# Kernel tuning notes

Measured on AMD Instinct MI355X. Metric: run time of the kernel, lower is better.

The kernel has to match this reference:

```python
import jax, jax.numpy as jnp
import numpy as np

N, K, D_IN, D_H, D_A, N_CLS = 8192, 10, 1024, 512, 256, 4


def setup_inputs() -> dict:
    key = jax.random.key(0)
    ks = jax.random.split(key, 20)
    def lin(k, fan_in, shape):
        return jax.random.normal(k, shape, dtype=jnp.float32) / np.sqrt(fan_in)
    return {
        "x_path": jax.random.normal(ks[0], (N, D_IN), dtype=jnp.float32),
        "cluster_id": jax.random.randint(ks[1], (N,), 0, K),
        # per-cluster phi MLP (Linear 1024->512, ReLU, Linear 512->512, ReLU); dropout = eval identity
        "W1": lin(ks[2], D_IN, (K, D_IN, D_H)), "b1": jnp.zeros((K, D_H), jnp.float32),
        "W2": lin(ks[3], D_H, (K, D_H, D_H)), "b2": jnp.zeros((K, D_H), jnp.float32),
        # attention_net fc: Linear 512->512 + ReLU
        "fc_W": lin(ks[4], D_H, (D_H, D_H)), "fc_b": jnp.zeros((D_H,), jnp.float32),
        # Attn_Net_Gated: a=tanh(Va), b=sigmoid(Vb), A=(a*b)@Vc
        "Va": lin(ks[5], D_H, (D_H, D_A)), "ba": jnp.zeros((D_A,), jnp.float32),
        "Vb": lin(ks[6], D_H, (D_H, D_A)), "bb": jnp.zeros((D_A,), jnp.float32),
        "Vc": lin(ks[7], D_A, (D_A, 1)), "bc": jnp.zeros((1,), jnp.float32),
        # rho: Linear 512->256 + ReLU
        "rho_W": lin(ks[8], D_H, (D_H, D_A)), "rho_b": jnp.zeros((D_A,), jnp.float32),
        # classifier: Linear 256->4
        "cls_W": lin(ks[9], D_A, (D_A, N_CLS)), "cls_b": jnp.zeros((N_CLS,), jnp.float32),
    }


def reference(x_path, cluster_id, W1, b1, W2, b2, fc_W, fc_b,
              Va, ba, Vb, bb, Vc, bc, rho_W, rho_b, cls_W, cls_b):
    # mask[k, n] = 1 if patch n belongs to cluster k
    mask = (cluster_id[None, :] == jnp.arange(K)[:, None]).astype(x_path.dtype)  # [K, N]

    # per-cluster 2-layer MLP applied to all patches, masked mean-pool (= AdaptiveAvgPool1d(1))
    def phi(W1i, b1i, W2i, b2i):
        h = jax.nn.relu(x_path @ W1i + b1i)          # [N, 512]
        return jax.nn.relu(h @ W2i + b2i)            # [N, 512]
    y = jax.vmap(phi)(W1, b1, W2, b2)                # [K, N, 512]
    cnt = mask.sum(axis=1)                           # [K]
    pooled = jnp.einsum('kn,knd->kd', mask, y) / jnp.maximum(cnt, 1.0)[:, None]  # [K, 512]
    # empty cluster -> zeros (matches torch.zeros((1,512)) branch since b terms are zero via where)
    pooled = jnp.where(cnt[:, None] > 0, pooled, 0.0)

    # attention_net: fc + gated attention
    h = jax.nn.relu(pooled @ fc_W + fc_b)            # [K, 512]
    a = jnp.tanh(h @ Va + ba)                        # [K, 256]
    b = jax.nn.sigmoid(h @ Vb + bb)                  # [K, 256]
    A = (a * b) @ Vc + bc                            # [K, 1]
    A = jax.nn.softmax(A.T, axis=1)                  # [1, K]
    h_path = A @ h                                   # [1, 512]
    h_path = jax.nn.relu(h_path @ rho_W + rho_b)[0]  # [256]
    logits = (h_path @ cls_W + cls_b)[None, :]       # [1, 4]
    Y_hat = jnp.argmax(logits, axis=1, keepdims=True)
    hazards = jax.nn.sigmoid(logits)
    S = jnp.cumprod(1.0 - hazards, axis=1)
    return hazards, S, Y_hat
```

## Files before the change

### kernel.cpp

```cpp
#include <hip/hip_runtime.h>
#include <math.h>

#define NPATCH 8192
#define KC     10
#define DIN    1024
#define DH     512
#define DA     256
#define NCLS   4

#define TM  32
#define LDA 520

typedef unsigned short u16;
typedef short bf16x8 __attribute__((ext_vector_type(8)));
typedef float f32x4  __attribute__((ext_vector_type(4)));

#define OFF_CNT   0
#define OFF_BAR   48
#define OFF_IDX   64
#define OFF_PSUM  327744
#define OFF_H     348224
#define OFF_H2    368768
#define OFF_SRED  369792
#define OFF_W1P   373888
#define OFF_W2P   10859648
#define OFF_H1    16102528

__device__ __forceinline__ u16 f2bf(float f) {
  union { float f; unsigned u; } v; v.f = f;
  unsigned r = (v.u + 0x7fffu + ((v.u >> 16) & 1u)) >> 16;
  return (u16)r;
}

struct __align__(8) U16x4 { u16 x, y, z, w; };

__device__ __forceinline__ void async16(const void* gp, void* lp) {
  __builtin_amdgcn_global_load_lds(
      (const __attribute__((address_space(1))) void*)gp,
      (__attribute__((address_space(3))) void*)lp, 16, 0, 0);
}

#define W1_TILES (KC * (DIN / 32) * (DH / 32))
#define W2_TILES (KC * (DH / 32) * (DH / 32))
#define NB_BUCKET 32
#define NB_PREP (NB_BUCKET + W1_TILES + W2_TILES)

__global__ __launch_bounds__(256) void prep_kernel(
    const int* __restrict__ cid, int* __restrict__ cnt,
    int* __restrict__ idxlist, const float* __restrict__ W1,
    const float* __restrict__ W2, u16* __restrict__ W1p,
    u16* __restrict__ W2p, float* __restrict__ psum) {
  int b = blockIdx.x, t = threadIdx.x;
  if (b < NB_BUCKET) {
    int g = b * 256 + t;
    if (g < KC * DH) psum[g] = 0.f;
    __shared__ int lcnt[KC], lbase[KC];
    if (t < KC) lcnt[t] = 0;
    __syncthreads();
    int n = b * 256 + t;
    int k = cid[n];
    int myoff = atomicAdd(&lcnt[k], 1);
    __syncthreads();
    if (t < KC) lbase[t] = atomicAdd(&cnt[t], lcnt[t]);
    __syncthreads();
    idxlist[k * NPATCH + lbase[k] + myoff] = n;
  } else {
    __shared__ u16 tile[32][33];
    int bb = b - NB_BUCKET;
    const float* src;
    u16* dst;
    if (bb < W1_TILES) {
      int k = bb / 512, rem = bb % 512;
      int kb = rem / 16, n0 = (rem % 16) * 32;
      src = W1 + (size_t)k * DIN * DH + (size_t)kb * 32 * DH + n0;
      dst = W1p + (((size_t)(k * 32 + kb) * 512 + n0) * 32);
    } else {
      int b2 = bb - W1_TILES;
      int k = b2 / 256, rem = b2 % 256;
      int kb = rem / 16, n0 = (rem % 16) * 32;
      src = W2 + (size_t)k * DH * DH + (size_t)kb * 32 * DH + n0;
      dst = W2p + (((size_t)(k * 16 + kb) * 512 + n0) * 32);
    }
    {
      int ki = t >> 3, n4 = (t & 7) * 4;
      float4 v = *(const float4*)&src[(size_t)ki * DH + n4];
      tile[ki][n4 + 0] = f2bf(v.x);
      tile[ki][n4 + 1] = f2bf(v.y);
      tile[ki][n4 + 2] = f2bf(v.z);
      tile[ki][n4 + 3] = f2bf(v.w);
    }
    __syncthreads();
    {
      int n = t >> 3, ki = (t & 7) * 4;
      U16x4 o = {tile[ki + 0][n], tile[ki + 1][n], tile[ki + 2][n],
                 tile[ki + 3][n]};
      *(U16x4*)&dst[(size_t)n * 32 + ki] = o;
    }
  }
}

__global__ __launch_bounds__(256) void phi1_kernel(
    const float* __restrict__ x, const u16* __restrict__ W1p,
    const float* __restrict__ b1, const int* __restrict__ cnt,
    const int* __restrict__ idxlist, u16* __restrict__ h1) {
  const int k = blockIdx.y;
  const int base = blockIdx.x * TM;
  const int nq = blockIdx.z;
  const int cntk = cnt[k];
  if (base >= cntk) return;

  const int tid = threadIdx.x;
  const int w = tid >> 6, lane = tid & 63;
  const int quad = lane >> 4, l16 = lane & 15;

  __shared__ __align__(16) u16 A_sh[TM * LDA];
  __shared__ int ridx[TM];
  if (tid < TM) {
    int r = base + tid;
    ridx[tid] = (r < cntk) ? idxlist[k * NPATCH + r] : -1;
  }
  __syncthreads();

  const f32x4 zero4 = {0.f, 0.f, 0.f, 0.f};
  f32x4 acc[2][4];
#pragma unroll
  for (int m = 0; m < 2; ++m)
#pragma unroll
    for (int nt = 0; nt < 4; ++nt) acc[m][nt] = zero4;

  for (int kh = 0; kh < 2; ++kh) {
    if (kh) __syncthreads();
#pragma unroll
    for (int rr = 0; rr < 8; ++rr) {
      int r = w * 8 + rr;
      int src = ridx[r];
      bf16x8 o = {0, 0, 0, 0, 0, 0, 0, 0};
      if (src >= 0) {
        const float4* xp =
            (const float4*)(x + (size_t)src * DIN + kh * 512 + lane * 8);
        float4 v0 = xp[0], v1 = xp[1];
        o[0] = (short)f2bf(v0.x); o[1] = (short)f2bf(v0.y);
        o[2] = (short)f2bf(v0.z); o[3] = (short)f2bf(v0.w);
        o[4] = (short)f2bf(v1.x); o[5] = (short)f2bf(v1.y);
        o[6] = (short)f2bf(v1.z); o[7] = (short)f2bf(v1.w);
      }
      *(bf16x8*)&A_sh[r * LDA + lane * 8] = o;
    }
    __syncthreads();

    const u16* wb = W1p + ((size_t)(k * 32 + kh * 16) * 512 +
                           (nq * 256 + w * 64 + l16)) * 32 + quad * 8;
    bf16x8 B[2][8];
#pragma unroll
    for (int s = 0; s < 2; ++s)
#pragma unroll
      for (int nt = 0; nt < 4; ++nt)
        B[0][s * 4 + nt] = *(const bf16x8*)(wb + (size_t)s * 16384 + nt * 512);
#pragma unroll
    for (int g = 0; g < 8; ++g) {
      const int cur = g & 1, nxt = cur ^ 1;
      if (g < 7) {
#pragma unroll
        for (int s = 0; s < 2; ++s)
#pragma unroll
          for (int nt = 0; nt < 4; ++nt)
            B[nxt][s * 4 + nt] = *(const bf16x8*)(
                wb + (size_t)((g + 1) * 2 + s) * 16384 + nt * 512);
      }
#pragma unroll
      for (int s = 0; s < 2; ++s) {
        const int ks = g * 2 + s;
        bf16x8 af0 = *(const bf16x8*)&A_sh[l16 * LDA + ks * 32 + quad * 8];
        bf16x8 af1 =
            *(const bf16x8*)&A_sh[(16 + l16) * LDA + ks * 32 + quad * 8];
#pragma unroll
        for (int nt = 0; nt < 4; ++nt) {
          acc[0][nt] = __builtin_amdgcn_mfma_f32_16x16x32_bf16(
              af0, B[cur][s * 4 + nt], acc[0][nt], 0, 0, 0);
          acc[1][nt] = __builtin_amdgcn_mfma_f32_16x16x32_bf16(
              af1, B[cur][s * 4 + nt], acc[1][nt], 0, 0, 0);
        }
      }
    }
  }

  __syncthreads();
#pragma unroll
  for (int m = 0; m < 2; ++m)
#pragma unroll
    for (int nt = 0; nt < 4; ++nt) {
      int c = w * 64 + nt * 16 + l16;
      float bias = b1[k * DH + nq * 256 + c];
#pragma unroll
      for (int r = 0; r < 4; ++r) {
        int row = m * 16 + quad * 4 + r;
        A_sh[row * 264 + c] = f2bf(fmaxf(acc[m][nt][r] + bias, 0.f));
      }
    }
  __syncthreads();
  {
    int row = tid >> 3, seg = tid & 7;
    int n = ridx[row];
    if (n >= 0) {
      u16* dst = h1 + (size_t)n * DH + nq * 256 + seg * 32;
#pragma unroll
      for (int j = 0; j < 4; ++j)
        *(bf16x8*)(dst + j * 8) =
            *(const bf16x8*)&A_sh[row * 264 + seg * 32 + j * 8];
    }
  }
}

__global__ __launch_bounds__(256) void phi2_kernel(
    const u16* __restrict__ h1, const u16* __restrict__ W2p,
    const float* __restrict__ b2, const int* __restrict__ cnt,
    const int* __restrict__ idxlist, float* __restrict__ psum) {
  const int k = blockIdx.y;
  const int base = blockIdx.x * TM;
  const int nq = blockIdx.z;
  const int cntk = cnt[k];
  if (base >= cntk) return;

  const int tid = threadIdx.x;
  const int w = tid >> 6, lane = tid & 63;
  const int quad = lane >> 4, l16 = lane & 15;

  __shared__ __align__(16) u16 H_sh[TM * LDA];
  __shared__ int ridx[TM];
  if (tid < TM) {
    int r = base + tid;
    ridx[tid] = (r < cntk) ? idxlist[k * NPATCH + r] : -1;
  }
  __syncthreads();

  for (int rr = 0; rr < 8; ++rr) {
    int r = w * 8 + rr;
    int src = ridx[r];
    if (src >= 0) {
      async16(h1 + (size_t)src * DH + lane * 8, &H_sh[r * LDA]);
    } else {
      bf16x8 z = {0, 0, 0, 0, 0, 0, 0, 0};
      *(bf16x8*)&H_sh[r * LDA + lane * 8] = z;
    }
  }
  __syncthreads();

  const f32x4 zero4 = {0.f, 0.f, 0.f, 0.f};
  f32x4 acc[2][4];
#pragma unroll
  for (int m = 0; m < 2; ++m)
#pragma unroll
    for (int nt = 0; nt < 4; ++nt) acc[m][nt] = zero4;

  const u16* wb = W2p + ((size_t)(k * 16) * 512 +
                         (nq * 256 + w * 64 + l16)) * 32 + quad * 8;
  bf16x8 B[2][8];
#pragma unroll
  for (int s = 0; s < 2; ++s)
#pragma unroll
    for (int nt = 0; nt < 4; ++nt)
      B[0][s * 4 + nt] = *(const bf16x8*)(wb + (size_t)s * 16384 + nt * 512);
#pragma unroll
  for (int g = 0; g < 8; ++g) {
    const int cur = g & 1, nxt = cur ^ 1;
    if (g < 7) {
#pragma unroll
      for (int s = 0; s < 2; ++s)
#pragma unroll
        for (int nt = 0; nt < 4; ++nt)
          B[nxt][s * 4 + nt] = *(const bf16x8*)(
              wb + (size_t)((g + 1) * 2 + s) * 16384 + nt * 512);
    }
#pragma unroll
    for (int s = 0; s < 2; ++s) {
      const int ks = g * 2 + s;
      bf16x8 af0 = *(const bf16x8*)&H_sh[l16 * LDA + ks * 32 + quad * 8];
      bf16x8 af1 =
          *(const bf16x8*)&H_sh[(16 + l16) * LDA + ks * 32 + quad * 8];
#pragma unroll
      for (int nt = 0; nt < 4; ++nt) {
        acc[0][nt] = __builtin_amdgcn_mfma_f32_16x16x32_bf16(
            af0, B[cur][s * 4 + nt], acc[0][nt], 0, 0, 0);
        acc[1][nt] = __builtin_amdgcn_mfma_f32_16x16x32_bf16(
            af1, B[cur][s * 4 + nt], acc[1][nt], 0, 0, 0);
      }
    }
  }

  float vmask[2][4];
#pragma unroll
  for (int m = 0; m < 2; ++m)
#pragma unroll
    for (int r = 0; r < 4; ++r)
      vmask[m][r] = (ridx[m * 16 + quad * 4 + r] >= 0) ? 1.f : 0.f;

#pragma unroll
  for (int nt = 0; nt < 4; ++nt) {
    int col = nq * 256 + w * 64 + nt * 16 + l16;
    float bias = b2[k * DH + col];
    float s = 0.f;
#pragma unroll
    for (int m = 0; m < 2; ++m)
#pragma unroll
      for (int r = 0; r < 4; ++r)
        s += vmask[m][r] * fmaxf(acc[m][nt][r] + bias, 0.f);
    s += __shfl_xor(s, 16, 64);
    s += __shfl_xor(s, 32, 64);
    if (quad == 0) atomicAdd(&psum[k * DH + col], s);
  }
}

#define NTB 64

__device__ __forceinline__ void bar_arrive_wait(int* bar) {
  __syncthreads();
  if (threadIdx.x == 0) {
    __threadfence();
    __hip_atomic_fetch_add(bar, 1, __ATOMIC_RELEASE, __HIP_MEMORY_SCOPE_AGENT);
    while (__hip_atomic_load(bar, __ATOMIC_ACQUIRE,
                             __HIP_MEMORY_SCOPE_AGENT) < NTB) {
      __builtin_amdgcn_s_sleep(1);
    }
  }
  __syncthreads();
}

__global__ __launch_bounds__(256) void tail_kernel(
    const float* __restrict__ psum, const int* __restrict__ cnt,
    const float* __restrict__ fcW, const float* __restrict__ fcb,
    const float* __restrict__ Va, const float* __restrict__ ba,
    const float* __restrict__ Vb, const float* __restrict__ bb_,
    const float* __restrict__ Vc, const float* __restrict__ rhoW,
    const float* __restrict__ rhob, const float* __restrict__ clsW,
    const float* __restrict__ clsb, float* __restrict__ hstore,
    float* __restrict__ sred, float* __restrict__ h2g,
    int* __restrict__ bar, float* __restrict__ out) {
  __shared__ float p_sh[KC * DH];
  __shared__ float r1[2560];
  __shared__ float r2[2560];
  __shared__ float invs[KC];
  __shared__ float gate_sh[4 * KC];
  __shared__ float ws_sh[KC];
  __shared__ float hp_sh[DH];
  const int tid = threadIdx.x;
  const int b = blockIdx.x;

  if (tid < KC) {
    int c = cnt[tid];
    invs[tid] = (c > 0) ? 1.f / (float)c : 0.f;
  }
  __syncthreads();
#pragma unroll
  for (int it = 0; it < KC * DH / 256; ++it) {
    int e = it * 256 + tid;
    p_sh[e] = psum[e] * invs[e >> 9];
  }
  __syncthreads();
  {
    const int jj = tid & 7, dq = tid >> 3;
    const int j0 = b * 8;
    float acc[KC];
#pragma unroll
    for (int k = 0; k < KC; ++k) acc[k] = 0.f;
#pragma unroll 4
    for (int i = 0; i < 16; ++i) {
      int d = dq * 16 + i;
      float wv = fcW[(size_t)d * DH + j0 + jj];
#pragma unroll
      for (int k = 0; k < KC; ++k) acc[k] = fmaf(p_sh[k * DH + d], wv, acc[k]);
    }
#pragma unroll
    for (int k = 0; k < KC; ++k) r1[(dq * 8 + jj) * KC + k] = acc[k];
    __syncthreads();
    if (tid < 8 * KC) {
      int jj2 = tid / KC, k = tid % KC;
      float s = 0.f;
#pragma unroll
      for (int q = 0; q < 32; ++q) s += r1[(q * 8 + jj2) * KC + k];
      hstore[k * DH + j0 + jj2] = fmaxf(s + fcb[j0 + jj2], 0.f);
    }
  }
  bar_arrive_wait(&bar[0]);

#pragma unroll
  for (int it = 0; it < KC * DH / 256; ++it) {
    int e = it * 256 + tid;
    p_sh[e] = hstore[e];
  }
  __syncthreads();
  {
    const int jj = tid & 3, dq = tid >> 2;
    const int j0 = b * 4;
    float sa[KC], sb[KC];
#pragma unroll
    for (int k = 0; k < KC; ++k) { sa[k] = 0.f; sb[k] = 0.f; }
#pragma unroll 4
    for (int i = 0; i < 8; ++i) {
      int d = dq * 8 + i;
      float va = Va[(size_t)d * DA + j0 + jj];
      float vb = Vb[(size_t)d * DA + j0 + jj];
#pragma unroll
      for (int k = 0; k < KC; ++k) {
        float h = p_sh[k * DH + d];
        sa[k] = fmaf(h, va, sa[k]);
        sb[k] = fmaf(h, vb, sb[k]);
      }
    }
#pragma unroll
    for (int k = 0; k < KC; ++k) {
      r1[(dq * 4 + jj) * KC + k] = sa[k];
      r2[(dq * 4 + jj) * KC + k] = sb[k];
    }
    __syncthreads();
    if (tid < 4 * KC) {
      int jj2 = tid / KC, k = tid % KC;
      float ta = 0.f, tb = 0.f;
#pragma unroll
      for (int q = 0; q < 64; ++q) {
        ta += r1[(q * 4 + jj2) * KC + k];
        tb += r2[(q * 4 + jj2) * KC + k];
      }
      float a = tanhf(ta + ba[j0 + jj2]);
      float g = 1.f / (1.f + expf(-(tb + bb_[j0 + jj2])));
      gate_sh[jj2 * KC + k] = a * g * Vc[j0 + jj2];
    }
    __syncthreads();
    if (tid < KC) {
      float s = 0.f;
#pragma unroll
      for (int jj2 = 0; jj2 < 4; ++jj2) s += gate_sh[jj2 * KC + tid];
      sred[b * 16 + tid] = s;
    }
  }
  bar_arrive_wait(&bar[1]);

  if (tid < KC) {
    float s = 0.f;
    for (int q = 0; q < NTB; ++q) s += sred[q * 16 + tid];
    ws_sh[tid] = s;
  }
  __syncthreads();
  if (tid == 0) {
    float m = -1e30f;
#pragma unroll
    for (int k2 = 0; k2 < KC; ++k2) m = fmaxf(m, ws_sh[k2]);
    float Z = 0.f;
#pragma unroll
    for (int k2 = 0; k2 < KC; ++k2) {
      float e = expf(ws_sh[k2] - m);
      ws_sh[k2] = e;
      Z += e;
    }
    float iZ = 1.f / Z;
#pragma unroll
    for (int k2 = 0; k2 < KC; ++k2) ws_sh[k2] *= iZ;
  }
  __syncthreads();
#pragma unroll
  for (int it = 0; it < 2; ++it) {
    int d = it * 256 + tid;
    float s = 0.f;
#pragma unroll
    for (int k2 = 0; k2 < KC; ++k2) s = fmaf(ws_sh[k2], p_sh[k2 * DH + d], s);
    hp_sh[d] = s;
  }
  __syncthreads();
  {
    const int jj = tid & 3, dq = tid >> 2;
    const int j0 = b * 4;
    float acc = 0.f;
#pragma unroll 4
    for (int i = 0; i < 8; ++i) {
      int d = dq * 8 + i;
      acc = fmaf(hp_sh[d], rhoW[(size_t)d * DA + j0 + jj], acc);
    }
    r1[dq * 4 + jj] = acc;
    __syncthreads();
    if (tid < 4) {
      float s = 0.f;
#pragma unroll
      for (int q = 0; q < 64; ++q) s += r1[q * 4 + tid];
      h2g[j0 + tid] = fmaxf(s + rhob[j0 + tid], 0.f);
    }
  }

  if (b != 0) {
    __syncthreads();
    if (tid == 0) {
      __threadfence();
      __hip_atomic_fetch_add(&bar[2], 1, __ATOMIC_RELEASE,
                             __HIP_MEMORY_SCOPE_AGENT);
    }
    return;
  }
  bar_arrive_wait(&bar[2]);
  {
    float h = h2g[tid];
#pragma unroll
    for (int c = 0; c < NCLS; ++c)
      r1[c * 256 + tid] = h * clsW[(size_t)tid * NCLS + c];
    __syncthreads();
    for (int s = 128; s > 0; s >>= 1) {
      if (tid < s) {
#pragma unroll
        for (int c = 0; c < NCLS; ++c)
          r1[c * 256 + tid] += r1[c * 256 + tid + s];
      }
      __syncthreads();
    }
    if (tid == 0) {
      float lg[NCLS], hz[NCLS];
      int best = 0;
#pragma unroll
      for (int c = 0; c < NCLS; ++c) {
        lg[c] = r1[c * 256] + clsb[c];
        hz[c] = 1.f / (1.f + expf(-lg[c]));
        if (lg[c] > lg[best]) best = c;
      }
      float S = 1.f;
#pragma unroll
      for (int c = 0; c < NCLS; ++c) out[c] = hz[c];
#pragma unroll
      for (int c = 0; c < NCLS; ++c) {
        S *= (1.f - hz[c]);
        out[NCLS + c] = S;
      }
      out[2 * NCLS] = (float)best;
    }
  }
}

extern "C" void kernel_launch(void* const* d_in, const int* in_sizes, int n_in,
                              void* d_out, int out_size, void* d_ws,
                              size_t ws_size, hipStream_t stream) {
  const float* x    = (const float*)d_in[0];
  const int*   cid  = (const int*)d_in[1];
  const float* W1   = (const float*)d_in[2];
  const float* b1   = (const float*)d_in[3];
  const float* W2   = (const float*)d_in[4];
  const float* b2   = (const float*)d_in[5];
  const float* fcW  = (const float*)d_in[6];
  const float* fcb  = (const float*)d_in[7];
  const float* Va   = (const float*)d_in[8];
  const float* ba   = (const float*)d_in[9];
  const float* Vb   = (const float*)d_in[10];
  const float* bb_  = (const float*)d_in[11];
  const float* Vc   = (const float*)d_in[12];
  const float* rhoW = (const float*)d_in[14];
  const float* rhob = (const float*)d_in[15];
  const float* clsW = (const float*)d_in[16];
  const float* clsb = (const float*)d_in[17];
  float* out = (float*)d_out;

  char* ws = (char*)d_ws;
  int*   cnt     = (int*)(ws + OFF_CNT);
  int*   bar     = (int*)(ws + OFF_BAR);
  int*   idxlist = (int*)(ws + OFF_IDX);
  float* psum    = (float*)(ws + OFF_PSUM);
  float* hstore  = (float*)(ws + OFF_H);
  float* h2g     = (float*)(ws + OFF_H2);
  float* sred    = (float*)(ws + OFF_SRED);
  u16*   W1p     = (u16*)(ws + OFF_W1P);
  u16*   W2p     = (u16*)(ws + OFF_W2P);
  u16*   h1      = (u16*)(ws + OFF_H1);

  (void)hipMemsetAsync(cnt, 0, 64, stream);
  prep_kernel<<<NB_PREP, 256, 0, stream>>>(cid, cnt, idxlist, W1, W2, W1p, W2p,
                                           psum);
  phi1_kernel<<<dim3(NPATCH / TM, KC, 2), 256, 0, stream>>>(x, W1p, b1, cnt,
                                                            idxlist, h1);
  phi2_kernel<<<dim3(NPATCH / TM, KC, 2), 256, 0, stream>>>(h1, W2p, b2, cnt,
                                                            idxlist, psum);
  tail_kernel<<<NTB, 256, 0, stream>>>(psum, cnt, fcW, fcb, Va, ba, Vb, bb_,
                                       Vc, rhoW, rhob, clsW, clsb, hstore,
                                       sred, h2g, bar, out);
}
```

Measured before the change: 215.2 us.

## Store h1 compacted by cluster, reorder grid, use packed bf16 converts

phi1 now writes h1 rows contiguously in cluster-sorted order, at a prefix-sum offset computed from the counts. phi2 therefore reads contiguous rows without the index-list gather, and it no longer needs the shared ridx table or its sync. The grid is reordered to (nq, k padded to 12, row-tile) so the two column halves of a tile launch next to each other, which should improve cache reuse of the x and h1 rows. The fp32-to-bf16 input conversion uses the hardware v_cvt_pk_bf16_f32 instruction in place of manual rounding. Padding the k dimension adds some empty blocks that exit early.

```diff
diff --git a/kernel.cpp b/kernel.cpp
--- a/kernel.cpp
+++ b/kernel.cpp
@@ -32,7 +32,14 @@
   return (u16)r;
 }
 
+__device__ __forceinline__ unsigned cvtpk(float lo, float hi) {
+  unsigned r;
+  asm("v_cvt_pk_bf16_f32 %0, %1, %2" : "=v"(r) : "v"(lo), "v"(hi));
+  return r;
+}
+
 struct __align__(8) U16x4 { u16 x, y, z, w; };
+union BF8U { bf16x8 v; unsigned u[4]; };
 
 __device__ __forceinline__ void async16(const void* gp, void* lp) {
   __builtin_amdgcn_global_load_lds(
@@ -104,10 +111,15 @@
     const float* __restrict__ b1, const int* __restrict__ cnt,
     const int* __restrict__ idxlist, u16* __restrict__ h1) {
   const int k = blockIdx.y;
-  const int base = blockIdx.x * TM;
-  const int nq = blockIdx.z;
+  if (k >= KC) return;
   const int cntk = cnt[k];
+  const int base = blockIdx.z * TM;
   if (base >= cntk) return;
+  const int nq = blockIdx.x;
+
+  int cbase = 0;
+#pragma unroll
+  for (int i = 0; i < KC - 1; ++i) cbase += (i < k) ? cnt[i] : 0;
 
   const int tid = threadIdx.x;
   const int w = tid >> 6, lane = tid & 63;
@@ -134,17 +146,19 @@
     for (int rr = 0; rr < 8; ++rr) {
       int r = w * 8 + rr;
       int src = ridx[r];
-      bf16x8 o = {0, 0, 0, 0, 0, 0, 0, 0};
+      BF8U o;
       if (src >= 0) {
         const float4* xp =
             (const float4*)(x + (size_t)src * DIN + kh * 512 + lane * 8);
         float4 v0 = xp[0], v1 = xp[1];
-        o[0] = (short)f2bf(v0.x); o[1] = (short)f2bf(v0.y);
-        o[2] = (short)f2bf(v0.z); o[3] = (short)f2bf(v0.w);
-        o[4] = (short)f2bf(v1.x); o[5] = (short)f2bf(v1.y);
-        o[6] = (short)f2bf(v1.z); o[7] = (short)f2bf(v1.w);
-      }
-      *(bf16x8*)&A_sh[r * LDA + lane * 8] = o;
+        o.u[0] = cvtpk(v0.x, v0.y);
+        o.u[1] = cvtpk(v0.z, v0.w);
+        o.u[2] = cvtpk(v1.x, v1.y);
+        o.u[3] = cvtpk(v1.z, v1.w);
+      } else {
+        o.u[0] = 0; o.u[1] = 0; o.u[2] = 0; o.u[3] = 0;
+      }
+      *(bf16x8*)&A_sh[r * LDA + lane * 8] = o.v;
     }
     __syncthreads();
 
@@ -200,9 +214,8 @@
   __syncthreads();
   {
     int row = tid >> 3, seg = tid & 7;
-    int n = ridx[row];
-    if (n >= 0) {
-      u16* dst = h1 + (size_t)n * DH + nq * 256 + seg * 32;
+    if (base + row < cntk) {
+      u16* dst = h1 + (size_t)(cbase + base + row) * DH + nq * 256 + seg * 32;
 #pragma unroll
       for (int j = 0; j < 4; ++j)
         *(bf16x8*)(dst + j * 8) =
@@ -214,30 +227,29 @@
 __global__ __launch_bounds__(256) void phi2_kernel(
     const u16* __restrict__ h1, const u16* __restrict__ W2p,
     const float* __restrict__ b2, const int* __restrict__ cnt,
-    const int* __restrict__ idxlist, float* __restrict__ psum) {
+    float* __restrict__ psum) {
   const int k = blockIdx.y;
-  const int base = blockIdx.x * TM;
-  const int nq = blockIdx.z;
+  if (k >= KC) return;
   const int cntk = cnt[k];
+  const int base = blockIdx.z * TM;
   if (base >= cntk) return;
+  const int nq = blockIdx.x;
+
+  int cbase = 0;
+#pragma unroll
+  for (int i = 0; i < KC - 1; ++i) cbase += (i < k) ? cnt[i] : 0;
 
   const int tid = threadIdx.x;
   const int w = tid >> 6, lane = tid & 63;
   const int quad = lane >> 4, l16 = lane & 15;
 
   __shared__ __align__(16) u16 H_sh[TM * LDA];
-  __shared__ int ridx[TM];
-  if (tid < TM) {
-    int r = base + tid;
-    ridx[tid] = (r < cntk) ? idxlist[k * NPATCH + r] : -1;
-  }
-  __syncthreads();
-
+
+  const int rowg0 = cbase + base;
   for (int rr = 0; rr < 8; ++rr) {
     int r = w * 8 + rr;
-    int src = ridx[r];
-    if (src >= 0) {
-      async16(h1 + (size_t)src * DH + lane * 8, &H_sh[r * LDA]);
+    if (base + r < cntk) {
+      async16(h1 + (size_t)(rowg0 + r) * DH + lane * 8, &H_sh[r * LDA]);
     } else {
       bf16x8 z = {0, 0, 0, 0, 0, 0, 0, 0};
       *(bf16x8*)&H_sh[r * LDA + lane * 8] = z;
@@ -292,7 +304,7 @@
   for (int m = 0; m < 2; ++m)
 #pragma unroll
     for (int r = 0; r < 4; ++r)
-      vmask[m][r] = (ridx[m * 16 + quad * 4 + r] >= 0) ? 1.f : 0.f;
+      vmask[m][r] = (base + m * 16 + quad * 4 + r < cntk) ? 1.f : 0.f;
 
 #pragma unroll
   for (int nt = 0; nt < 4; ++nt) {
@@ -567,10 +579,10 @@
   (void)hipMemsetAsync(cnt, 0, 64, stream);
   prep_kernel<<<NB_PREP, 256, 0, stream>>>(cid, cnt, idxlist, W1, W2, W1p, W2p,
                                            psum);
-  phi1_kernel<<<dim3(NPATCH / TM, KC, 2), 256, 0, stream>>>(x, W1p, b1, cnt,
+  phi1_kernel<<<dim3(2, 12, NPATCH / TM), 256, 0, stream>>>(x, W1p, b1, cnt,
                                                             idxlist, h1);
-  phi2_kernel<<<dim3(NPATCH / TM, KC, 2), 256, 0, stream>>>(h1, W2p, b2, cnt,
-                                                            idxlist, psum);
+  phi2_kernel<<<dim3(2, 12, NPATCH / TM), 256, 0, stream>>>(h1, W2p, b2, cnt,
+                                                            psum);
   tail_kernel<<<NTB, 256, 0, stream>>>(psum, cnt, fcW, fcb, Va, ba, Vb, bb_,
                                        Vc, rhoW, rhob, clsW, clsb, hstore,
                                        sred, h2g, bar, out);
```

New measurement: 206.3 us. 4.1% less time.
